# Kernel optimization log

Hardware: AMD Instinct MI355X
Metric: run time of the kernel (lower is better)

The kernel has to match this reference:

```python
import jax, jax.numpy as jnp
import numpy as np

# HMS2 tiling configuration (matches init_kwargs)
TILE = 512          # tile_size in image pixels
CROP = 8            # emb_crop_size (in embedding pixels)
STRIDE = 4          # emb_stride_size: total downsampling of conv_module
OVERLAP = CROP * STRIDE * 2          # 64 image pixels
STEP = TILE - OVERLAP                # 448: stride between tile origins
IMG = 2304                           # image H = W; (IMG-TILE) % STEP == 0
NT = (IMG - TILE) // STEP + 1        # 5 tiles per axis
B = 1
E = TILE // STRIDE                   # 128: emb pixels per (uncropped) tile
DN = ('NHWC', 'HWIO', 'NHWC')


def conv_module(x, W1, b1, W2, b2):
    # Two stride-2 SAME convs with ReLU: total stride 4 (= emb_stride_size).
    x = jax.lax.conv_general_dilated(x, W1, (2, 2), 'SAME', dimension_numbers=DN) + b1
    x = jax.nn.relu(x)
    x = jax.lax.conv_general_dilated(x, W2, (2, 2), 'SAME', dimension_numbers=DN) + b2
    return jax.nn.relu(x)


def setup_inputs() -> dict:
    key = jax.random.key(0)
    k1, k2, k3 = jax.random.split(key, 3)
    image_batch = jax.random.randint(k1, (B, IMG, IMG, 3), 0, 256, dtype=jnp.int32)
    W1 = jax.random.normal(k2, (3, 3, 3, 64), dtype=jnp.float32) * 0.05
    b1 = jnp.zeros((64,), dtype=jnp.float32)
    W2 = jax.random.normal(k3, (3, 3, 64, 128), dtype=jnp.float32) * 0.05
    b2 = jnp.zeros((128,), dtype=jnp.float32)
    return {'image_batch': image_batch, 'W1': W1, 'b1': b1, 'W2': W2, 'b2': b2}


def reference(image_batch, W1, b1, W2, b2):
    # loader_module: slice tile from the big uint8 NHWC image, normalize to float.
    img = image_batch.astype(jnp.float32) / 255.0
    # Extract all overlapping tiles (static slices) -> [NT*NT, B, TILE, TILE, 3]
    tiles = jnp.stack([img[:, ty * STEP:ty * STEP + TILE, tx * STEP:tx * STEP + TILE, :]
                       for ty in range(NT) for tx in range(NT)])
    tiles = tiles.reshape(NT * NT * B, TILE, TILE, 3)
    emb = conv_module(tiles, W1, b1, W2, b2)          # [NT*NT*B, E, E, 128]
    emb = emb.reshape(NT, NT, B, E, E, -1)
    # Crop emb_crop_size on interior edges and stitch (as in _forward_tile).
    rows = []
    for ty in range(NT):
        top = 0 if ty == 0 else CROP
        bot = E if ty == NT - 1 else E - CROP
        cols = []
        for tx in range(NT):
            left = 0 if tx == 0 else CROP
            right = E if tx == NT - 1 else E - CROP
            cols.append(emb[ty, tx][:, top:bot, left:right, :])
        rows.append(jnp.concatenate(cols, axis=2))
    out = jnp.concatenate(rows, axis=1)               # [B, 576, 576, 128] NHWC
    return jnp.transpose(out, (0, 3, 1, 2))           # NCHW, matching torch emb
```

## Files before the change

kernel.cpp:

```cpp
#include <hip/hip_runtime.h>


#define IMG 2304
#define H1  1152
#define H2  576
#define C1  64
#define C2  128
#define TS  8
#define NTB (H2/TS)
#define C1T 17
#define IT  35

typedef __bf16 bf16_t;
typedef __bf16 bf16x8 __attribute__((ext_vector_type(8)));
typedef __bf16 bf16x4 __attribute__((ext_vector_type(4)));
typedef _Float16 f16_t;
typedef _Float16 f16x8 __attribute__((ext_vector_type(8)));
typedef float  f32x16 __attribute__((ext_vector_type(16)));

#define W2T_BYTES (C2*576*2)

#define SWZ(s, g) ( (((s)>>1)*128) + (((((g) + (((s)&1)<<2) + (((s)>>1)&7)) & 7)) << 4) )

__global__ __launch_bounds__(256) void w2_transform(
    const float* __restrict__ W2, bf16_t* __restrict__ W2T)
{
    int idx = blockIdx.x*256 + threadIdx.x;
    int e   = idx & 7;
    int t   = idx >> 3;
    int n   = t & 127;  t >>= 7;
    int oct = t & 3;    t >>= 2;
    int kykx= t % 9;
    int p   = t / 9;
    int chh = oct >> 1, kg = oct & 1;
    int ci64 = p*32 + chh*16 + kg*8 + e;
    W2T[idx] = (bf16_t)W2[(size_t)(kykx*64 + ci64)*C2 + n];
}

__global__ __launch_bounds__(64) void w1_transform(
    const float* __restrict__ W1, const float* __restrict__ b1,
    f16_t* __restrict__ W1T)
{
    int oc = threadIdx.x;
    for (int k = 0; k < 32; ++k) {
        float v = 0.f;
        if (k < 27) v = W1[k*C1 + oc];
        else if (k == 27) v = b1[oc];
        W1T[oc*32 + k] = (f16_t)v;
    }
}

__global__ __launch_bounds__(256, 4) void hms2_fused(
    const int*    __restrict__ img,
    const float*  __restrict__ b2,
    const bf16_t* __restrict__ W2T,
    const f16_t*  __restrict__ W1T,
    float*        __restrict__ out)
{
    __shared__ __align__(16) char s_raw[39040];
    char*  s_i2cb = s_raw;
    float* s_img  = (float*)(s_raw + 20480);
    char*  s_c1b  = s_raw + 20480;
    float* s_ep   = (float*)s_raw;

    const int tid   = threadIdx.x;
    const int tileY = blockIdx.x / NTB;
    const int tileX = blockIdx.x % NTB;
    const int e0y = tileY*TS, e0x = tileX*TS;
    const int r0  = 2*e0y,    q0  = 2*e0x;
    const int iy0 = 4*e0y,    ix0 = 4*e0x;

    for (int i = tid; i < IT*IT*3; i += 256) {
        int ch = i % 3, pp = i / 3;
        int r = pp / IT, c = pp % IT;
        int gy = iy0 + r, gx = ix0 + c;
        float v = 0.f;
        if (gy < IMG && gx < IMG)
            v = (float)img[((size_t)gy*IMG + gx)*3 + ch] * (1.f/255.f);
        s_img[i] = v;
    }

    const int kcol = tid & 31;
    const int ky_ = kcol/9, krem = kcol - 9*ky_;
    const int kx_ = krem/3, ic_  = krem - 3*kx_;
    const int koff  = ky_*(IT*3) + kx_*3 + ic_;
    const bool kReal = (kcol < 27), kIs27 = (kcol == 27);

    __syncthreads();

    for (int idx = tid; idx < 320*32; idx += 256) {
        int s = idx >> 5;
        f16_t v = (f16_t)0.f;
        if (s < 289) {
            int r = s/17, q = s - 17*r;
            if (kReal)      v = (f16_t)s_img[(2*r*IT + 2*q)*3 + koff];
            else if (kIs27) v = (f16_t)1.f;
        }
        *(f16_t*)(s_i2cb + SWZ(s, kcol>>3) + (kcol&7)*2) = v;
    }

    const int lane = tid & 63;
    const int m    = lane & 31;
    const int kg   = lane >> 5;
    const int cg   = __builtin_amdgcn_readfirstlane(tid >> 6);

    const int h0  = m >> 3, w0 = m & 7;
    const int s00 = 34*h0 + 2*w0;
    const bf16_t* bBase = W2T + (size_t)kg*1024 + (size_t)(cg*32 + m)*8;

    f32x16 acc0, acc1;
    #pragma unroll
    for (int r = 0; r < 16; ++r) { acc0[r] = 0.f; acc1[r] = 0.f; }

    __syncthreads();

    #pragma unroll 1
    for (int p = 0; p < 2; ++p) {
        const f16_t* w1p = W1T + (size_t)(p*32 + m)*32 + kg*8;
        f16x8 wA = *(const f16x8*)(w1p);
        f16x8 wB = *(const f16x8*)(w1p + 16);

        for (int sf = cg; sf < 10; sf += 4) {
            const int s = sf*32 + m;
            f16x8 i0 = *(const f16x8*)(s_i2cb + SWZ(s, kg));
            f16x8 i1 = *(const f16x8*)(s_i2cb + SWZ(s, kg+2));
            f32x16 d;
            #pragma unroll
            for (int r = 0; r < 16; ++r) d[r] = 0.f;
            d = __builtin_amdgcn_mfma_f32_32x32x16_f16(wA, i0, d, 0, 0, 0);
            d = __builtin_amdgcn_mfma_f32_32x32x16_f16(wB, i1, d, 0, 0, 0);

            if (s < 289) {
                int rsp = s/17, qsp = s - 17*rsp;
                bool ok = (r0 + rsp < H1) && (q0 + qsp < H1);
                #pragma unroll
                for (int g = 0; g < 4; ++g) {
                    bf16x4 vv;
                    #pragma unroll
                    for (int jj = 0; jj < 4; ++jj) {
                        float x = fmaxf(d[4*g + jj], 0.f);
                        vv[jj] = ok ? (bf16_t)x : (bf16_t)0.f;
                    }
                    *(bf16x4*)(s_c1b + SWZ(s, g) + kg*8) = vv;
                }
            }
        }
        __syncthreads();

        const bf16_t* bP = bBase + (size_t)p*36*1024;
        #pragma unroll
        for (int kk = 0; kk < 9; ++kk) {
            const int dsh = (kk/3)*17 + (kk - 3*(kk/3));
            const int sA0 = s00 + dsh;
            const int sA1 = sA0 + 136;
            #pragma unroll
            for (int chh = 0; chh < 2; ++chh) {
                bf16x8 aF0 = *(const bf16x8*)(s_c1b + SWZ(sA0, 2*chh + kg));
                bf16x8 aF1 = *(const bf16x8*)(s_c1b + SWZ(sA1, 2*chh + kg));
                bf16x8 bF  = *(const bf16x8*)(bP + (size_t)(kk*4 + chh*2)*1024);
                acc0 = __builtin_amdgcn_mfma_f32_32x32x16_bf16(aF0, bF, acc0, 0, 0, 0);
                acc1 = __builtin_amdgcn_mfma_f32_32x32x16_bf16(aF1, bF, acc1, 0, 0, 0);
            }
        }
        __syncthreads();
    }

    {
        const int cOut = cg*32 + m;
        const float b2v = b2[cOut];
        #pragma unroll
        for (int r = 0; r < 16; ++r) {
            int row = (r&3) + 8*(r>>2) + 4*kg;
            s_ep[cOut*67 + row]      = fmaxf(acc0[r] + b2v, 0.f);
            s_ep[cOut*67 + 32 + row] = fmaxf(acc1[r] + b2v, 0.f);
        }
        __syncthreads();
        const int sp = tid & 63;
        const int gy = e0y + (sp >> 3), gx = e0x + (sp & 7);
        #pragma unroll
        for (int j = 0; j < 32; ++j) {
            int c = cg*32 + j;
            out[(size_t)c*(H2*H2) + (size_t)gy*H2 + gx] = s_ep[c*67 + sp];
        }
    }
}

extern "C" void kernel_launch(void* const* d_in, const int* in_sizes, int n_in,
                              void* d_out, int out_size, void* d_ws, size_t ws_size,
                              hipStream_t stream) {
    const int*   img = (const int*)  d_in[0];
    const float* W1  = (const float*)d_in[1];
    const float* b1  = (const float*)d_in[2];
    const float* W2  = (const float*)d_in[3];
    const float* b2  = (const float*)d_in[4];
    float*       out = (float*)d_out;
    bf16_t*      W2T = (bf16_t*)d_ws;
    f16_t*       W1T = (f16_t*)((char*)d_ws + W2T_BYTES);

    w2_transform<<<dim3(288), dim3(256), 0, stream>>>(W2, W2T);
    w1_transform<<<dim3(1),   dim3(64),  0, stream>>>(W1, b1, W1T);
    hms2_fused<<<dim3(NTB*NTB), dim3(256), 0, stream>>>(img, b2, W2T, W1T, out);
}
```

Baseline: 386.2 us.

## Drop im2col staging, read conv1 operands from fp16 image rows, halve epilogue LDS

The separate fp32 image staging and swizzled im2col buffer are replaced by a compact fp16 row-major image tile. MFMA operands for conv1 are gathered directly from it using a reordered W1 layout, where each k-group covers contiguous row segments. The epilogue is split into two channel halves so a smaller LDS footprint suffices, and launch bounds are raised to 6 blocks per CU. The two weight-transform kernels are merged into one launch with coalesced reads of W2. In exchange, the epilogue gains an extra barrier and the conv1 operand loads become unaligned scalar LDS reads.

```diff
diff --git a/kernel.cpp b/kernel.cpp
--- a/kernel.cpp
+++ b/kernel.cpp
@@ -10,6 +10,8 @@
 #define NTB (H2/TS)
 #define C1T 17
 #define IT  35
+#define IRS 212
+#define C1OFF 7424
 
 typedef __bf16 bf16_t;
 typedef __bf16 bf16x8 __attribute__((ext_vector_type(8)));
@@ -17,51 +19,52 @@
 typedef _Float16 f16_t;
 typedef _Float16 f16x8 __attribute__((ext_vector_type(8)));
 typedef float  f32x16 __attribute__((ext_vector_type(16)));
+typedef unsigned int uint32;
+typedef uint32 u32x4 __attribute__((ext_vector_type(4)));
 
 #define W2T_BYTES (C2*576*2)
 
 #define SWZ(s, g) ( (((s)>>1)*128) + (((((g) + (((s)&1)<<2) + (((s)>>1)&7)) & 7)) << 4) )
 
-__global__ __launch_bounds__(256) void w2_transform(
-    const float* __restrict__ W2, bf16_t* __restrict__ W2T)
+__global__ __launch_bounds__(256) void weights_transform(
+    const float* __restrict__ W2, const float* __restrict__ W1,
+    const float* __restrict__ b1,
+    bf16_t* __restrict__ W2T, f16_t* __restrict__ W1T)
 {
-    int idx = blockIdx.x*256 + threadIdx.x;
-    int e   = idx & 7;
-    int t   = idx >> 3;
-    int n   = t & 127;  t >>= 7;
-    int oct = t & 3;    t >>= 2;
-    int kykx= t % 9;
-    int p   = t / 9;
-    int chh = oct >> 1, kg = oct & 1;
-    int ci64 = p*32 + chh*16 + kg*8 + e;
-    W2T[idx] = (bf16_t)W2[(size_t)(kykx*64 + ci64)*C2 + n];
+    if (blockIdx.x < 288) {
+        int src = blockIdx.x*256 + threadIdx.x;
+        int n = src & 127, ci = (src >> 7) & 63, kykx = src >> 13;
+        int p = ci >> 5, chh = (ci >> 4) & 1, kg = (ci >> 3) & 1, e = ci & 7;
+        W2T[((((p*9 + kykx) << 2) + (chh << 1) + kg) << 10) + (n << 3) + e]
+            = (bf16_t)W2[src];
+    } else {
+        int t = threadIdx.x;
+        int oc = t & 63, grp = t >> 6;
+        #pragma unroll
+        for (int j = 0; j < 8; ++j) {
+            int kh = grp*8 + j;
+            float v;
+            if (kh < 24)       v = W1[(9*(kh >> 3) + (kh & 7))*C1 + oc];
+            else if (kh == 24) v = W1[ 8*C1 + oc];
+            else if (kh == 25) v = W1[17*C1 + oc];
+            else if (kh == 26) v = W1[26*C1 + oc];
+            else if (kh == 27) v = b1[oc];
+            else               v = 0.f;
+            W1T[oc*32 + kh] = (f16_t)v;
+        }
+    }
 }
 
-__global__ __launch_bounds__(64) void w1_transform(
-    const float* __restrict__ W1, const float* __restrict__ b1,
-    f16_t* __restrict__ W1T)
-{
-    int oc = threadIdx.x;
-    for (int k = 0; k < 32; ++k) {
-        float v = 0.f;
-        if (k < 27) v = W1[k*C1 + oc];
-        else if (k == 27) v = b1[oc];
-        W1T[oc*32 + k] = (f16_t)v;
-    }
-}
-
-__global__ __launch_bounds__(256, 4) void hms2_fused(
+__global__ __launch_bounds__(256, 6) void hms2_fused(
     const int*    __restrict__ img,
     const float*  __restrict__ b2,
     const bf16_t* __restrict__ W2T,
     const f16_t*  __restrict__ W1T,
     float*        __restrict__ out)
 {
-    __shared__ __align__(16) char s_raw[39040];
-    char*  s_i2cb = s_raw;
-    float* s_img  = (float*)(s_raw + 20480);
-    char*  s_c1b  = s_raw + 20480;
-    float* s_ep   = (float*)s_raw;
+    __shared__ __align__(16) char s_raw[25984];
+    char*  s_c1b = s_raw + C1OFF;
+    float* s_ep  = (float*)s_raw;
 
     const int tid   = threadIdx.x;
     const int tileY = blockIdx.x / NTB;
@@ -70,33 +73,13 @@
     const int r0  = 2*e0y,    q0  = 2*e0x;
     const int iy0 = 4*e0y,    ix0 = 4*e0x;
 
-    for (int i = tid; i < IT*IT*3; i += 256) {
-        int ch = i % 3, pp = i / 3;
-        int r = pp / IT, c = pp % IT;
-        int gy = iy0 + r, gx = ix0 + c;
+    const int cb = ix0*3;
+    for (int i = tid; i < 35*105; i += 256) {
+        int r = i/105, w = i - 105*r;
         float v = 0.f;
-        if (gy < IMG && gx < IMG)
-            v = (float)img[((size_t)gy*IMG + gx)*3 + ch] * (1.f/255.f);
-        s_img[i] = v;
-    }
-
-    const int kcol = tid & 31;
-    const int ky_ = kcol/9, krem = kcol - 9*ky_;
-    const int kx_ = krem/3, ic_  = krem - 3*kx_;
-    const int koff  = ky_*(IT*3) + kx_*3 + ic_;
-    const bool kReal = (kcol < 27), kIs27 = (kcol == 27);
-
-    __syncthreads();
-
-    for (int idx = tid; idx < 320*32; idx += 256) {
-        int s = idx >> 5;
-        f16_t v = (f16_t)0.f;
-        if (s < 289) {
-            int r = s/17, q = s - 17*r;
-            if (kReal)      v = (f16_t)s_img[(2*r*IT + 2*q)*3 + koff];
-            else if (kIs27) v = (f16_t)1.f;
-        }
-        *(f16_t*)(s_i2cb + SWZ(s, kcol>>3) + (kcol&7)*2) = v;
+        if ((iy0 + r < IMG) && (cb + w < IMG*3))
+            v = (float)img[(size_t)(iy0 + r)*(IMG*3) + cb + w] * (1.f/255.f);
+        *(f16_t*)(s_raw + r*IRS + 2*w) = (f16_t)v;
     }
 
     const int lane = tid & 63;
@@ -122,17 +105,40 @@
 
         for (int sf = cg; sf < 10; sf += 4) {
             const int s = sf*32 + m;
-            f16x8 i0 = *(const f16x8*)(s_i2cb + SWZ(s, kg));
-            f16x8 i1 = *(const f16x8*)(s_i2cb + SWZ(s, kg+2));
+            const int r = s/17, q = s - 17*r;
+            const int base = r*(2*IRS) + 12*q;
+            u32x4 f1, f2;
+            {
+                const char* rb = s_raw + base + kg*IRS;
+                f1.x = *(const uint32*)(rb);
+                f1.y = *(const uint32*)(rb + 4);
+                f1.z = *(const uint32*)(rb + 8);
+                f1.w = *(const uint32*)(rb + 12);
+            }
+            if (kg == 0) {
+                const char* rc = s_raw + base + 2*IRS;
+                f2.x = *(const uint32*)(rc);
+                f2.y = *(const uint32*)(rc + 4);
+                f2.z = *(const uint32*)(rc + 8);
+                f2.w = *(const uint32*)(rc + 12);
+            } else {
+                uint32 a  = *(const unsigned short*)(s_raw + base + 16);
+                uint32 bb = *(const unsigned short*)(s_raw + base + IRS + 16);
+                uint32 cc = *(const unsigned short*)(s_raw + base + 2*IRS + 16);
+                f2.x = a | (bb << 16);
+                f2.y = cc | (0x3C00u << 16);
+                f2.z = 0; f2.w = 0;
+            }
+            f16x8 i0 = __builtin_bit_cast(f16x8, f1);
+            f16x8 i1 = __builtin_bit_cast(f16x8, f2);
             f32x16 d;
             #pragma unroll
-            for (int r = 0; r < 16; ++r) d[r] = 0.f;
+            for (int rr = 0; rr < 16; ++rr) d[rr] = 0.f;
             d = __builtin_amdgcn_mfma_f32_32x32x16_f16(wA, i0, d, 0, 0, 0);
             d = __builtin_amdgcn_mfma_f32_32x32x16_f16(wB, i1, d, 0, 0, 0);
 
             if (s < 289) {
-                int rsp = s/17, qsp = s - 17*rsp;
-                bool ok = (r0 + rsp < H1) && (q0 + qsp < H1);
+                bool ok = (r0 + r < H1) && (q0 + q < H1);
                 #pragma unroll
                 for (int g = 0; g < 4; ++g) {
                     bf16x4 vv;
@@ -168,19 +174,28 @@
     {
         const int cOut = cg*32 + m;
         const float b2v = b2[cOut];
-        #pragma unroll
-        for (int r = 0; r < 16; ++r) {
-            int row = (r&3) + 8*(r>>2) + 4*kg;
-            s_ep[cOut*67 + row]      = fmaxf(acc0[r] + b2v, 0.f);
-            s_ep[cOut*67 + 32 + row] = fmaxf(acc1[r] + b2v, 0.f);
-        }
-        __syncthreads();
         const int sp = tid & 63;
-        const int gy = e0y + (sp >> 3), gx = e0x + (sp & 7);
-        #pragma unroll
-        for (int j = 0; j < 32; ++j) {
-            int c = cg*32 + j;
-            out[(size_t)c*(H2*H2) + (size_t)gy*H2 + gx] = s_ep[c*67 + sp];
+        const int gyE = e0y + (sp >> 3), gxE = e0x + (sp & 7);
+        const int c0 = tid >> 6;
+        #pragma unroll 1
+        for (int hf = 0; hf < 2; ++hf) {
+            if ((cg >> 1) == hf) {
+                const int cl = (cg & 1)*32 + m;
+                #pragma unroll
+                for (int r = 0; r < 16; ++r) {
+                    int row = (r&3) + 8*(r>>2) + 4*kg;
+                    s_ep[cl*66 + row]      = fmaxf(acc0[r] + b2v, 0.f);
+                    s_ep[cl*66 + 32 + row] = fmaxf(acc1[r] + b2v, 0.f);
+                }
+            }
+            __syncthreads();
+            #pragma unroll
+            for (int j = 0; j < 16; ++j) {
+                int cl = c0 + 4*j;
+                out[(size_t)(hf*64 + cl)*(H2*H2) + (size_t)gyE*H2 + gxE]
+                    = s_ep[cl*66 + sp];
+            }
+            if (hf == 0) __syncthreads();
         }
     }
 }
@@ -197,7 +212,6 @@
     bf16_t*      W2T = (bf16_t*)d_ws;
     f16_t*       W1T = (f16_t*)((char*)d_ws + W2T_BYTES);
 
-    w2_transform<<<dim3(288), dim3(256), 0, stream>>>(W2, W2T);
-    w1_transform<<<dim3(1),   dim3(64),  0, stream>>>(W1, b1, W1T);
+    weights_transform<<<dim3(289), dim3(256), 0, stream>>>(W2, W1, b1, W2T, W1T);
     hms2_fused<<<dim3(NTB*NTB), dim3(256), 0, stream>>>(img, b2, W2T, W1T, out);
 }
```

Result: slower. 469.9 us (+21.7%).
